# Optimization experiments

Measured on AMD Instinct MI355X. Metric: run time of the kernel, lower is better.

## Reference

```python
import jax, jax.numpy as jnp
import numpy as np

EPS = 1e-5  # torch BatchNorm default eps
B_SEG = 64
PTS_PER_SEG = 16384
N_TOTAL = B_SEG * PTS_PER_SEG
D_IN = 32
D_OUT = 64


def setup_inputs() -> dict:
    key = jax.random.key(0)
    k = jax.random.split(key, 4)
    x = jax.random.normal(k[0], (N_TOTAL, D_IN), dtype=jnp.float32)
    length = jnp.full((B_SEG,), PTS_PER_SEG, dtype=jnp.int32)
    # conv1d_1: Conv1d(32, 1, 1) -> weight [1,32,1], bias [1]; flatten to vector/scalar
    w1 = jax.random.normal(k[1], (D_IN,), dtype=jnp.float32) * 0.1
    b1 = jnp.zeros((), dtype=jnp.float32)
    # bn_1: BatchNorm1d(1)
    g1 = jnp.ones((), dtype=jnp.float32)
    beta1 = jnp.zeros((), dtype=jnp.float32)
    # fc_1: Linear(32, 64)
    W2 = jax.random.normal(k[2], (D_IN, D_OUT), dtype=jnp.float32) * 0.05
    b2 = jnp.zeros((D_OUT,), dtype=jnp.float32)
    # bn_2: BatchNorm1d(64)
    g2 = jnp.ones((D_OUT,), dtype=jnp.float32)
    beta2 = jnp.zeros((D_OUT,), dtype=jnp.float32)
    return {"x": x, "length": length, "w1": w1, "b1": b1, "g1": g1,
            "beta1": beta1, "W2": W2, "b2": b2, "g2": g2, "beta2": beta2}


def reference(x, length, w1, b1, g1, beta1, W2, b2, g2, beta2):
    N = x.shape[0]
    B = length.shape[0]
    # conv1d(32->1, k=1) over all N points: per-point scalar score
    z = x @ w1 + b1                                        # [N]
    # BatchNorm1d(1) in training mode: stats over all N points (biased var)
    mu = jnp.mean(z)
    var = jnp.var(z)
    out1 = g1 * (z - mu) * jax.lax.rsqrt(var + EPS) + beta1  # [N]

    # segment ids from ragged lengths (total length is static)
    seg = jnp.repeat(jnp.arange(B, dtype=jnp.int32), length,
                     total_repeat_length=N)                 # [N]

    # sft = mean(x * out1[:,None], axis=1), softmax per segment
    s = jnp.mean(x * out1[:, None], axis=1)                 # [N]
    smax = jax.ops.segment_max(s, seg, num_segments=B)      # [B]
    e = jnp.exp(s - smax[seg])                              # [N]
    denom = jax.ops.segment_sum(e, seg, num_segments=B)     # [B]
    w = e / denom[seg]                                      # [N] softmax weights

    # temp = mean over segment of (x * w)  (mean, not weighted sum)
    pooled = jax.ops.segment_sum(x * w[:, None], seg, num_segments=B)
    pooled = pooled / length[:, None].astype(x.dtype)       # [B, 32]

    # fc + BatchNorm1d(64) in training mode (stats over B rows)
    h = pooled @ W2 + b2                                    # [B, 64]
    mu2 = jnp.mean(h, axis=0)
    var2 = jnp.var(h, axis=0)
    out = g2 * (h - mu2) * jax.lax.rsqrt(var2 + EPS) + beta2
    return out
```

## Files before the change

### kernel.cpp

```cpp
#include <hip/hip_runtime.h>


#define EPS 1e-5f
#define NSB 2048
#define CHUNKS 32

#define WS_DPART   0
#define WS_OFFS    32768
#define WS_GNUM    33280
#define WS_GDEN    41472

__global__ __launch_bounds__(256, 8) void k_stats(const float* __restrict__ x,
                                                  const float* __restrict__ w1,
                                                  const float* __restrict__ b1,
                                                  const int* __restrict__ length,
                                                  int N, int B,
                                                  double* __restrict__ dpart,
                                                  int* __restrict__ offs,
                                                  float* __restrict__ gnum,
                                                  float* __restrict__ gden) {
    const int tid = threadIdx.x;

    if (blockIdx.x == 0) {
        for (int i = tid; i < B * 32; i += 256) gnum[i] = 0.f;
        for (int i = tid; i < B; i += 256) gden[i] = 0.f;
        __shared__ int slen[256];
        for (int i = tid; i < B; i += 256) slen[i] = length[i];
        __syncthreads();
        if (tid == 0) {
            int o = 0;
            offs[0] = 0;
            for (int bb = 0; bb < B; ++bb) { o += slen[bb]; offs[bb + 1] = o; }
        }
    }

    const int q = tid & 7;
    const float4 wq = ((const float4*)w1)[q];
    const float b1v = b1[0];
    const float4* __restrict__ xv = (const float4*)x;

    double accZ = 0.0, accZZ = 0.0;
    const int stride = gridDim.x * 32;
    for (int row = blockIdx.x * 32 + (tid >> 3); row < N; row += stride) {
        float4 v = xv[(size_t)row * 8 + q];
        float zp = v.x * wq.x;
        zp = fmaf(v.y, wq.y, zp);
        zp = fmaf(v.z, wq.z, zp);
        zp = fmaf(v.w, wq.w, zp);
        zp += __shfl_xor(zp, 1);
        zp += __shfl_xor(zp, 2);
        zp += __shfl_xor(zp, 4);
        if (q == 0) {
            double z = (double)(zp + b1v);
            accZ  += z;
            accZZ += z * z;
        }
    }

    __shared__ double sZ[256], sZZ[256];
    sZ[tid] = accZ; sZZ[tid] = accZZ;
    __syncthreads();
    for (int s = 128; s > 0; s >>= 1) {
        if (tid < s) { sZ[tid] += sZ[tid + s]; sZZ[tid] += sZZ[tid + s]; }
        __syncthreads();
    }
    if (tid == 0) {
        dpart[2 * blockIdx.x]     = sZ[0];
        dpart[2 * blockIdx.x + 1] = sZZ[0];
    }
}

__global__ __launch_bounds__(256, 8) void k_pool(const float* __restrict__ x,
                                                 const float* __restrict__ w1,
                                                 const float* __restrict__ b1,
                                                 const float* __restrict__ g1,
                                                 const float* __restrict__ beta1,
                                                 const double* __restrict__ dpart,
                                                 const int* __restrict__ offs,
                                                 int N,
                                                 float* __restrict__ gnum,
                                                 float* __restrict__ gden) {
    const int tid = threadIdx.x;

    __shared__ double sZ[256], sZZ[256];
    double aZ = 0.0, aZZ = 0.0;
    const double2* __restrict__ dp2 = (const double2*)dpart;
    for (int i = tid; i < NSB; i += 256) {
        double2 d = dp2[i];
        aZ += d.x; aZZ += d.y;
    }
    sZ[tid] = aZ; sZZ[tid] = aZZ;
    __syncthreads();
    for (int s = 128; s > 0; s >>= 1) {
        if (tid < s) { sZ[tid] += sZ[tid + s]; sZZ[tid] += sZZ[tid + s]; }
        __syncthreads();
    }
    __shared__ float cb[2];
    if (tid == 0) {
        double mu  = sZ[0] / (double)N;
        double var = sZZ[0] / (double)N - mu * mu;
        float c1 = (float)((double)g1[0] / sqrt(var + (double)EPS));
        cb[0] = c1;
        cb[1] = beta1[0] - (float)(c1 * mu);
    }
    __syncthreads();
    const float c1 = cb[0], c2 = cb[1];

    const int b   = blockIdx.y;
    const int off = offs[b];
    const int len = offs[b + 1] - off;
    const int rpc = (len + CHUNKS - 1) / CHUNKS;
    const int r0  = blockIdx.x * rpc;
    const int r1  = min(r0 + rpc, len);

    const int q = tid & 7;
    const float4 wq = ((const float4*)w1)[q];
    const float b1v = b1[0];
    const float4* __restrict__ xv = (const float4*)x;

    float4 acc = make_float4(0.f, 0.f, 0.f, 0.f);
    float accE = 0.f;

    for (int r = r0 + (tid >> 3); r < r1; r += 32) {
        float4 v = xv[(size_t)(off + r) * 8 + q];
        float zp = v.x * wq.x;
        zp = fmaf(v.y, wq.y, zp);
        zp = fmaf(v.z, wq.z, zp);
        zp = fmaf(v.w, wq.w, zp);
        float mp = v.x + v.y + v.z + v.w;
        zp += __shfl_xor(zp, 1);  mp += __shfl_xor(mp, 1);
        zp += __shfl_xor(zp, 2);  mp += __shfl_xor(mp, 2);
        zp += __shfl_xor(zp, 4);  mp += __shfl_xor(mp, 4);
        float s = fmaf(c1, zp + b1v, c2) * mp * 0.03125f;
        float e = __expf(s);
        acc.x = fmaf(e, v.x, acc.x);
        acc.y = fmaf(e, v.y, acc.y);
        acc.z = fmaf(e, v.z, acc.z);
        acc.w = fmaf(e, v.w, acc.w);
        if (q == 0) accE += e;
    }

#pragma unroll
    for (int msk = 8; msk < 64; msk <<= 1) {
        acc.x += __shfl_xor(acc.x, msk);
        acc.y += __shfl_xor(acc.y, msk);
        acc.z += __shfl_xor(acc.z, msk);
        acc.w += __shfl_xor(acc.w, msk);
        accE  += __shfl_xor(accE,  msk);
    }

    __shared__ float sred[4][33];
    const int wave = tid >> 6;
    const int lane = tid & 63;
    if (lane < 8) {
        sred[wave][4 * lane + 0] = acc.x;
        sred[wave][4 * lane + 1] = acc.y;
        sred[wave][4 * lane + 2] = acc.z;
        sred[wave][4 * lane + 3] = acc.w;
        if (lane == 0) sred[wave][32] = accE;
    }
    __syncthreads();
    if (tid < 33) {
        float s = sred[0][tid] + sred[1][tid] + sred[2][tid] + sred[3][tid];
        if (tid < 32) atomicAdd(&gnum[b * 32 + tid], s);
        else          atomicAdd(&gden[b], s);
    }
}

__global__ __launch_bounds__(256) void k_head(const float* __restrict__ gnum,
                                              const float* __restrict__ gden,
                                              const int* __restrict__ length,
                                              const float* __restrict__ W2,
                                              const float* __restrict__ b2,
                                              const float* __restrict__ g2,
                                              const float* __restrict__ beta2,
                                              float* __restrict__ out, int B) {
    __shared__ float pooled[64 * 32];
    __shared__ float h[64 * 64];
    __shared__ float mu2[64], isd[64];
    const int tid = threadIdx.x;

    for (int i = tid; i < B * 32; i += 256) {
        int bb = i >> 5;
        pooled[i] = gnum[i] / (gden[bb] * (float)length[bb]);
    }
    __syncthreads();

    const int j = tid & 63;
    const int g = tid >> 6;
    for (int r = 0; r < 16; ++r) {
        int bb = g * 16 + r;
        if (bb < B) {
            float hv = b2[j];
            for (int k = 0; k < 32; ++k) hv += pooled[bb * 32 + k] * W2[k * 64 + j];
            h[bb * 64 + j] = hv;
        }
    }
    __syncthreads();

    if (tid < 64) {
        float m = 0.f;
        for (int bb = 0; bb < B; ++bb) m += h[bb * 64 + tid];
        m /= (float)B;
        float v = 0.f;
        for (int bb = 0; bb < B; ++bb) { float d = h[bb * 64 + tid] - m; v += d * d; }
        v /= (float)B;
        mu2[tid] = m;
        isd[tid] = rsqrtf(v + EPS);
    }
    __syncthreads();

    for (int r = 0; r < 16; ++r) {
        int bb = g * 16 + r;
        if (bb < B) {
            int idx = bb * 64 + j;
            out[idx] = g2[j] * (h[idx] - mu2[j]) * isd[j] + beta2[j];
        }
    }
}

extern "C" void kernel_launch(void* const* d_in, const int* in_sizes, int n_in,
                              void* d_out, int out_size, void* d_ws, size_t ws_size,
                              hipStream_t stream) {
    const float* x      = (const float*)d_in[0];
    const int*   length = (const int*)  d_in[1];
    const float* w1     = (const float*)d_in[2];
    const float* b1     = (const float*)d_in[3];
    const float* g1     = (const float*)d_in[4];
    const float* beta1  = (const float*)d_in[5];
    const float* W2     = (const float*)d_in[6];
    const float* b2     = (const float*)d_in[7];
    const float* g2     = (const float*)d_in[8];
    const float* beta2  = (const float*)d_in[9];
    float* out = (float*)d_out;

    const int N = in_sizes[0] / 32;
    const int B = in_sizes[1];

    char* ws = (char*)d_ws;
    double* dpart  = (double*)(ws + WS_DPART);
    int*    offs   = (int*)   (ws + WS_OFFS);
    float*  gnum   = (float*) (ws + WS_GNUM);
    float*  gden   = (float*) (ws + WS_GDEN);

    k_stats<<<NSB, 256, 0, stream>>>(x, w1, b1, length, N, B, dpart, offs, gnum, gden);
    k_pool <<<dim3(CHUNKS, B), 256, 0, stream>>>(x, w1, b1, g1, beta1, dpart, offs, N,
                                                 gnum, gden);
    k_head <<<1, 256, 0, stream>>>(gnum, gden, length, W2, b2, g2, beta2, out, B);
}
```

Before: 246.5 us.

## Fuse stats finalize and head into last-block-done epilogues

Uses atomic counters so the last k_stats block reduces the partial sums and writes the BN1 constants once, removing the per-block redundant 2048-entry reduction in every k_pool block. The last k_pool block then runs the fc+BN2 head, so the separate k_head launch goes away. This adds a memset launch, atomic counters and threadfences, and lowers k_pool's occupancy hint because of the larger shared buffer.

```diff
diff --git a/kernel.cpp b/kernel.cpp
--- a/kernel.cpp
+++ b/kernel.cpp
@@ -5,17 +5,23 @@
 #define NSB 2048
 #define CHUNKS 32
 
-#define WS_DPART   0
-#define WS_OFFS    32768
-#define WS_GNUM    33280
-#define WS_GDEN    41472
+#define WS_CNT     0
+#define WS_DPART   16
+#define WS_CONSTS  32784
+#define WS_OFFS    32800
+#define WS_GNUM    33064
+#define WS_GDEN    41256
 
 __global__ __launch_bounds__(256, 8) void k_stats(const float* __restrict__ x,
                                                   const float* __restrict__ w1,
                                                   const float* __restrict__ b1,
+                                                  const float* __restrict__ g1,
+                                                  const float* __restrict__ beta1,
                                                   const int* __restrict__ length,
                                                   int N, int B,
+                                                  int* __restrict__ cnt,
                                                   double* __restrict__ dpart,
+                                                  float* __restrict__ consts,
                                                   int* __restrict__ offs,
                                                   float* __restrict__ gnum,
                                                   float* __restrict__ gden) {
@@ -64,47 +70,57 @@
         if (tid < s) { sZ[tid] += sZ[tid + s]; sZZ[tid] += sZZ[tid + s]; }
         __syncthreads();
     }
+
+    __shared__ int isLast;
     if (tid == 0) {
         dpart[2 * blockIdx.x]     = sZ[0];
         dpart[2 * blockIdx.x + 1] = sZZ[0];
+        __threadfence();
+        isLast = (atomicAdd(cnt, 1) == (int)gridDim.x - 1);
+    }
+    __syncthreads();
+
+    if (isLast) {
+        __threadfence();
+        double aZ = 0.0, aZZ = 0.0;
+        const double2* __restrict__ dp2 = (const double2*)dpart;
+        for (int i = tid; i < NSB; i += 256) {
+            double2 d = dp2[i];
+            aZ += d.x; aZZ += d.y;
+        }
+        sZ[tid] = aZ; sZZ[tid] = aZZ;
+        __syncthreads();
+        for (int s = 128; s > 0; s >>= 1) {
+            if (tid < s) { sZ[tid] += sZ[tid + s]; sZZ[tid] += sZZ[tid + s]; }
+            __syncthreads();
+        }
+        if (tid == 0) {
+            double mu  = sZ[0] / (double)N;
+            double var = sZZ[0] / (double)N - mu * mu;
+            float c1 = (float)((double)g1[0] / sqrt(var + (double)EPS));
+            consts[0] = c1;
+            consts[1] = beta1[0] - (float)(c1 * mu);
+        }
     }
 }
 
-__global__ __launch_bounds__(256, 8) void k_pool(const float* __restrict__ x,
+__global__ __launch_bounds__(256, 4) void k_pool(const float* __restrict__ x,
                                                  const float* __restrict__ w1,
                                                  const float* __restrict__ b1,
-                                                 const float* __restrict__ g1,
-                                                 const float* __restrict__ beta1,
-                                                 const double* __restrict__ dpart,
+                                                 const float* __restrict__ consts,
                                                  const int* __restrict__ offs,
-                                                 int N,
+                                                 const int* __restrict__ length,
+                                                 const float* __restrict__ W2,
+                                                 const float* __restrict__ b2,
+                                                 const float* __restrict__ g2,
+                                                 const float* __restrict__ beta2,
+                                                 int* __restrict__ cnt,
                                                  float* __restrict__ gnum,
-                                                 float* __restrict__ gden) {
+                                                 float* __restrict__ gden,
+                                                 float* __restrict__ out,
+                                                 int B) {
     const int tid = threadIdx.x;
-
-    __shared__ double sZ[256], sZZ[256];
-    double aZ = 0.0, aZZ = 0.0;
-    const double2* __restrict__ dp2 = (const double2*)dpart;
-    for (int i = tid; i < NSB; i += 256) {
-        double2 d = dp2[i];
-        aZ += d.x; aZZ += d.y;
-    }
-    sZ[tid] = aZ; sZZ[tid] = aZZ;
-    __syncthreads();
-    for (int s = 128; s > 0; s >>= 1) {
-        if (tid < s) { sZ[tid] += sZ[tid + s]; sZZ[tid] += sZZ[tid + s]; }
-        __syncthreads();
-    }
-    __shared__ float cb[2];
-    if (tid == 0) {
-        double mu  = sZ[0] / (double)N;
-        double var = sZZ[0] / (double)N - mu * mu;
-        float c1 = (float)((double)g1[0] / sqrt(var + (double)EPS));
-        cb[0] = c1;
-        cb[1] = beta1[0] - (float)(c1 * mu);
-    }
-    __syncthreads();
-    const float c1 = cb[0], c2 = cb[1];
+    const float c1 = consts[0], c2 = consts[1];
 
     const int b   = blockIdx.y;
     const int off = offs[b];
@@ -149,36 +165,38 @@
         accE  += __shfl_xor(accE,  msk);
     }
 
-    __shared__ float sred[4][33];
+    __shared__ float shead[64 * 32 + 64 * 64 + 128];
+    float* sred = shead;
     const int wave = tid >> 6;
     const int lane = tid & 63;
     if (lane < 8) {
-        sred[wave][4 * lane + 0] = acc.x;
-        sred[wave][4 * lane + 1] = acc.y;
-        sred[wave][4 * lane + 2] = acc.z;
-        sred[wave][4 * lane + 3] = acc.w;
-        if (lane == 0) sred[wave][32] = accE;
+        sred[wave * 33 + 4 * lane + 0] = acc.x;
+        sred[wave * 33 + 4 * lane + 1] = acc.y;
+        sred[wave * 33 + 4 * lane + 2] = acc.z;
+        sred[wave * 33 + 4 * lane + 3] = acc.w;
+        if (lane == 0) sred[wave * 33 + 32] = accE;
     }
     __syncthreads();
     if (tid < 33) {
-        float s = sred[0][tid] + sred[1][tid] + sred[2][tid] + sred[3][tid];
+        float s = sred[0 * 33 + tid] + sred[1 * 33 + tid] +
+                  sred[2 * 33 + tid] + sred[3 * 33 + tid];
         if (tid < 32) atomicAdd(&gnum[b * 32 + tid], s);
         else          atomicAdd(&gden[b], s);
-    }
-}
-
-__global__ __launch_bounds__(256) void k_head(const float* __restrict__ gnum,
-                                              const float* __restrict__ gden,
-                                              const int* __restrict__ length,
-                                              const float* __restrict__ W2,
-                                              const float* __restrict__ b2,
-                                              const float* __restrict__ g2,
-                                              const float* __restrict__ beta2,
-                                              float* __restrict__ out, int B) {
-    __shared__ float pooled[64 * 32];
-    __shared__ float h[64 * 64];
-    __shared__ float mu2[64], isd[64];
-    const int tid = threadIdx.x;
+        __threadfence();
+    }
+    __syncthreads();
+
+    __shared__ int isLast;
+    if (tid == 0)
+        isLast = (atomicAdd(cnt, 1) == (int)(gridDim.x * gridDim.y) - 1);
+    __syncthreads();
+    if (!isLast) return;
+
+    __threadfence();
+    float* pooled = shead;
+    float* h      = shead + 64 * 32;
+    float* mu2    = shead + 64 * 32 + 64 * 64;
+    float* isd    = mu2 + 64;
 
     for (int i = tid; i < B * 32; i += 256) {
         int bb = i >> 5;
@@ -238,13 +256,18 @@
     const int B = in_sizes[1];
 
     char* ws = (char*)d_ws;
+    int*    cnt    = (int*)   (ws + WS_CNT);
     double* dpart  = (double*)(ws + WS_DPART);
+    float*  consts = (float*) (ws + WS_CONSTS);
     int*    offs   = (int*)   (ws + WS_OFFS);
     float*  gnum   = (float*) (ws + WS_GNUM);
     float*  gden   = (float*) (ws + WS_GDEN);
 
-    k_stats<<<NSB, 256, 0, stream>>>(x, w1, b1, length, N, B, dpart, offs, gnum, gden);
-    k_pool <<<dim3(CHUNKS, B), 256, 0, stream>>>(x, w1, b1, g1, beta1, dpart, offs, N,
-                                                 gnum, gden);
-    k_head <<<1, 256, 0, stream>>>(gnum, gden, length, W2, b2, g2, beta2, out, B);
+    hipMemsetAsync(cnt, 0, 16, stream);
+
+    k_stats<<<NSB, 256, 0, stream>>>(x, w1, b1, g1, beta1, length, N, B,
+                                     cnt + 0, dpart, consts, offs, gnum, gden);
+    k_pool <<<dim3(CHUNKS, B), 256, 0, stream>>>(x, w1, b1, consts, offs, length,
+                                                 W2, b2, g2, beta2, cnt + 1,
+                                                 gnum, gden, out, B);
 }
```

Result: slower. 335.2 us (+36.0%).
